# Kernel optimization log

Hardware: AMD Instinct MI355X
Metric: run time of the kernel (lower is better)

The kernel has to match this reference:

```python
import jax, jax.numpy as jnp
import numpy as np
from jax import lax

LENGTH = 9
PAD = LENGTH // 2          # 4
WIN_SIZE = LENGTH * LENGTH # 81
EPS = 1e-09
ALPHA = 0.01
PENALTY = 'l2'


def setup_inputs() -> dict:
    key = jax.random.key(0)
    k1, k2, k3 = jax.random.split(key, 3)
    B, C, H, W = 8, 1, 1024, 1024
    I = jax.random.normal(k1, (B, C, H, W), dtype=jnp.float32)
    J = jax.random.normal(k2, (B, C, H, W), dtype=jnp.float32)
    s = jax.random.normal(k3, (B, 2, H, W), dtype=jnp.float32)
    # buffer: all-ones box filter, shape [out=1, in=C, k, k]
    sum_filt = jnp.ones((1, C, LENGTH, LENGTH), dtype=jnp.float32)
    return {"I": I, "J": J, "s": s, "sum_filt": sum_filt}


def _box_conv(x, filt):
    # NCHW conv with 'same' padding (odd kernel), stride 1 -> [B,1,H,W]
    return lax.conv_general_dilated(
        x, filt, window_strides=(1, 1),
        padding=[(PAD, PAD), (PAD, PAD)],
        dimension_numbers=('NCHW', 'OIHW', 'NCHW'))


def _compute_local_sums(I, J, filt):
    I2, J2, IJ = I * I, J * J, I * J
    I_sum = _box_conv(I, filt)
    J_sum = _box_conv(J, filt)
    I2_sum = _box_conv(I2, filt)
    J2_sum = _box_conv(J2, filt)
    IJ_sum = _box_conv(IJ, filt)
    u_I = I_sum / WIN_SIZE
    u_J = J_sum / WIN_SIZE
    cross = IJ_sum - u_J * I_sum - u_I * J_sum + u_I * u_J * WIN_SIZE
    I_var = I2_sum - 2 * u_I * I_sum + u_I * u_I * WIN_SIZE
    J_var = J2_sum - 2 * u_J * J_sum + u_J * u_J * WIN_SIZE
    return I_var, J_var, cross


def _gradient_loss(s):
    dy = jnp.abs(s[:, :, 1:, :] - s[:, :, :-1, :])
    dx = jnp.abs(s[:, :, :, 1:] - s[:, :, :, :-1])
    if PENALTY == 'l2':
        dy = dy * dy
        dx = dx * dx
    return (jnp.mean(dx) + jnp.mean(dy)) / 2.0


def reference(I, J, s, sum_filt):
    I_var, J_var, cross = _compute_local_sums(I, J, sum_filt)
    cc = cross * cross / (I_var * J_var + EPS)
    ncc_loss = -jnp.mean(cc)
    smoothness_loss = _gradient_loss(s) * ALPHA
    total_loss = ncc_loss + smoothness_loss
    return (total_loss, ncc_loss, smoothness_loss)
```

## Files before the change

kernel.cpp:

```cpp
#include <hip/hip_runtime.h>

#define HH 1024
#define WW 1024
#define NB 8
#define TY 8
#define NCC_BLOCKS (NB * (HH / TY))
#define SROWS 16
#define SM_BLOCKS (NB * 2 * HH / SROWS)
#define RW (1.0f / 81.0f)

template <int SGN>
__device__ __forceinline__ void vrow(const float* __restrict__ Ib, const float* __restrict__ Jb,
                                     int y, int t,
                                     float vI[4], float vJ[4],
                                     float vI2[4], float vJ2[4], float vIJ[4]) {
    if (y < 0 || y >= HH) return;
    const float4 i4 = ((const float4*)(Ib + (size_t)y * WW))[t];
    const float4 j4 = ((const float4*)(Jb + (size_t)y * WW))[t];
    const float fi[4] = {i4.x, i4.y, i4.z, i4.w};
    const float fj[4] = {j4.x, j4.y, j4.z, j4.w};
#pragma unroll
    for (int c = 0; c < 4; ++c) {
        const float a = fi[c], b = fj[c];
        if (SGN > 0) {
            vI[c] += a; vJ[c] += b;
            vI2[c] = fmaf(a, a, vI2[c]);
            vJ2[c] = fmaf(b, b, vJ2[c]);
            vIJ[c] = fmaf(a, b, vIJ[c]);
        } else {
            vI[c] -= a; vJ[c] -= b;
            vI2[c] = fmaf(-a, a, vI2[c]);
            vJ2[c] = fmaf(-b, b, vJ2[c]);
            vIJ[c] = fmaf(-a, b, vIJ[c]);
        }
    }
}

__device__ __forceinline__ void hslide(const float4 l, const float4 r, const float own[4], float hs[4]) {
    float h = l.x + l.y + l.z + l.w + own[0] + own[1] + own[2] + own[3] + r.x;
    hs[0] = h;
    h += r.y - l.x; hs[1] = h;
    h += r.z - l.y; hs[2] = h;
    h += r.w - l.z; hs[3] = h;
}

__global__ __launch_bounds__(256) void fused_kernel(const float* __restrict__ I,
                                                    const float* __restrict__ J,
                                                    const float* __restrict__ S,
                                                    float* __restrict__ ws) {
    __shared__ float4 cs[5][258];
    __shared__ float red[8];
    const int bid = blockIdx.x;
    const int t = threadIdx.x;
    const int lane = t & 63;
    const int wid = t >> 6;

    if ((bid & 1) == 0) {
        const int nb = bid >> 1;
        const int b = nb >> 7;
        const int strip = nb & 127;
        const int y0 = strip * TY;
        const float* Ib = I + (size_t)b * HH * WW;
        const float* Jb = J + (size_t)b * HH * WW;

        float vI[4] = {0, 0, 0, 0}, vJ[4] = {0, 0, 0, 0};
        float vI2[4] = {0, 0, 0, 0}, vJ2[4] = {0, 0, 0, 0}, vIJ[4] = {0, 0, 0, 0};
        float ccacc = 0.f;

        if (t < 5) {
            cs[t][0] = float4{0, 0, 0, 0};
            cs[t][257] = float4{0, 0, 0, 0};
        }

#pragma unroll
        for (int k = 0; k < 8; ++k)
            vrow<1>(Ib, Jb, y0 - 4 + k, t, vI, vJ, vI2, vJ2, vIJ);

#pragma unroll 2
        for (int k = 0; k < TY; ++k) {
            const int y = y0 + k;
            vrow<1>(Ib, Jb, y + 4, t, vI, vJ, vI2, vJ2, vIJ);

            cs[0][t + 1] = float4{vI[0], vI[1], vI[2], vI[3]};
            cs[1][t + 1] = float4{vJ[0], vJ[1], vJ[2], vJ[3]};
            cs[2][t + 1] = float4{vI2[0], vI2[1], vI2[2], vI2[3]};
            cs[3][t + 1] = float4{vJ2[0], vJ2[1], vJ2[2], vJ2[3]};
            cs[4][t + 1] = float4{vIJ[0], vIJ[1], vIJ[2], vIJ[3]};
            __syncthreads();

            float hsI[4], hsJ[4], hsI2[4], hsJ2[4], hsIJ[4];
            hslide(cs[0][t], cs[0][t + 2], vI, hsI);
            hslide(cs[1][t], cs[1][t + 2], vJ, hsJ);
            hslide(cs[2][t], cs[2][t + 2], vI2, hsI2);
            hslide(cs[3][t], cs[3][t + 2], vJ2, hsJ2);
            hslide(cs[4][t], cs[4][t + 2], vIJ, hsIJ);
            __syncthreads();

#pragma unroll
            for (int c = 0; c < 4; ++c) {
                const float Is = hsI[c], Js = hsJ[c];
                const float cross = fmaf(-Is * Js, RW, hsIJ[c]);
                const float Iv = fmaf(-Is * Is, RW, hsI2[c]);
                const float Jv = fmaf(-Js * Js, RW, hsJ2[c]);
                const float den = fmaf(Iv, Jv, 1e-9f);
                ccacc += cross * cross * __builtin_amdgcn_rcpf(den);
            }

            vrow<-1>(Ib, Jb, y - 4, t, vI, vJ, vI2, vJ2, vIJ);
        }

#pragma unroll
        for (int o = 32; o; o >>= 1) ccacc += __shfl_down(ccacc, o);
        if (lane == 0) red[wid] = ccacc;
        __syncthreads();
        if (t == 0) ws[nb] = red[0] + red[1] + red[2] + red[3];
    } else {
        const int sb = bid >> 1;
        const int r0 = sb * SROWS;
        const float* base = S + (size_t)r0 * WW;
        float dxacc = 0.f, dyacc = 0.f;

        float4 v = ((const float4*)base)[t];
#pragma unroll 2
        for (int k = 0; k < SROWS; ++k) {
            const int y = (r0 + k) & (HH - 1);
            const float* rp = base + (size_t)k * WW;
            const float d0 = v.y - v.x, d1 = v.z - v.y, d2 = v.w - v.z;
            dxacc += d0 * d0 + d1 * d1 + d2 * d2;
            if (t < 255) { const float vr = rp[4 * t + 4]; const float d3 = vr - v.w; dxacc += d3 * d3; }
            if (y < HH - 1) {
                const float4 vn = ((const float4*)(rp + WW))[t];
                const float e0 = vn.x - v.x, e1 = vn.y - v.y, e2 = vn.z - v.z, e3 = vn.w - v.w;
                dyacc += e0 * e0 + e1 * e1 + e2 * e2 + e3 * e3;
                v = vn;
            }
        }

#pragma unroll
        for (int o = 32; o; o >>= 1) {
            dxacc += __shfl_down(dxacc, o);
            dyacc += __shfl_down(dyacc, o);
        }
        if (lane == 0) { red[wid] = dxacc; red[4 + wid] = dyacc; }
        __syncthreads();
        if (t == 0) {
            ws[NCC_BLOCKS + sb] = red[0] + red[1] + red[2] + red[3];
            ws[NCC_BLOCKS + SM_BLOCKS + sb] = red[4] + red[5] + red[6] + red[7];
        }
    }
}

__global__ __launch_bounds__(256) void finalize_kernel(const float* __restrict__ ws,
                                                       float* __restrict__ out) {
    __shared__ double sd[256];
    __shared__ double res[3];
    const int t = threadIdx.x;
    double cc = 0.0, dx = 0.0, dy = 0.0;
    for (int i = t; i < NCC_BLOCKS; i += 256) cc += (double)ws[i];
    for (int i = t; i < SM_BLOCKS; i += 256) dx += (double)ws[NCC_BLOCKS + i];
    for (int i = t; i < SM_BLOCKS; i += 256) dy += (double)ws[NCC_BLOCKS + SM_BLOCKS + i];

    sd[t] = cc; __syncthreads();
    for (int s = 128; s; s >>= 1) { if (t < s) sd[t] += sd[t + s]; __syncthreads(); }
    if (t == 0) res[0] = sd[0];
    __syncthreads();
    sd[t] = dx; __syncthreads();
    for (int s = 128; s; s >>= 1) { if (t < s) sd[t] += sd[t + s]; __syncthreads(); }
    if (t == 0) res[1] = sd[0];
    __syncthreads();
    sd[t] = dy; __syncthreads();
    for (int s = 128; s; s >>= 1) { if (t < s) sd[t] += sd[t + s]; __syncthreads(); }
    if (t == 0) {
        res[2] = sd[0];
        const double ncc = -(res[0] / ((double)NB * 1.0 * HH * WW));
        const double mdx = res[1] / ((double)NB * 2.0 * HH * (WW - 1));
        const double mdy = res[2] / ((double)NB * 2.0 * (HH - 1) * WW);
        const double smooth = 0.01 * 0.5 * (mdx + mdy);
        out[0] = (float)(ncc + smooth);
        out[1] = (float)ncc;
        out[2] = (float)smooth;
    }
}

extern "C" void kernel_launch(void* const* d_in, const int* in_sizes, int n_in,
                              void* d_out, int out_size, void* d_ws, size_t ws_size,
                              hipStream_t stream) {
    const float* I = (const float*)d_in[0];
    const float* J = (const float*)d_in[1];
    const float* S = (const float*)d_in[2];
    float* ws = (float*)d_ws;
    float* out = (float*)d_out;

    fused_kernel<<<NCC_BLOCKS + SM_BLOCKS, 256, 0, stream>>>(I, J, S, ws);
    finalize_kernel<<<1, 256, 0, stream>>>(ws, out);
}
```

Baseline: 182.5 us.

## Give each wave a full row strip with 16 columns per lane and shuffle halos

Each 64-lane wave now owns a whole 1024-column row strip of its own, with 16 columns per lane, instead of a 256-thread block sharing one strip. The horizontal 9-wide sums use wave shuffles for the halo columns in place of shared-memory column sums and two block barriers per row. The strip height drops to 4 rows and the grid interleaves NCC and smoothness blocks 2:1. Vertical halo re-reads per strip grow relative to useful rows, and register pressure rises because each lane keeps 80 accumulators.

```diff
diff --git a/kernel.cpp b/kernel.cpp
--- a/kernel.cpp
+++ b/kernel.cpp
@@ -3,136 +3,181 @@
 #define HH 1024
 #define WW 1024
 #define NB 8
-#define TY 8
-#define NCC_BLOCKS (NB * (HH / TY))
-#define SROWS 16
-#define SM_BLOCKS (NB * 2 * HH / SROWS)
+#define TY 4
+#define NCC_WAVES (NB * (HH / TY))
+#define NCC_BLOCKS (NCC_WAVES / 4)
+#define SM_BLOCKS 256
+#define GRID (NCC_BLOCKS + SM_BLOCKS)
 #define RW (1.0f / 81.0f)
 
 template <int SGN>
-__device__ __forceinline__ void vrow(const float* __restrict__ Ib, const float* __restrict__ Jb,
-                                     int y, int t,
-                                     float vI[4], float vJ[4],
-                                     float vI2[4], float vJ2[4], float vIJ[4]) {
+__device__ __forceinline__ void vrow16(const float* __restrict__ Ib, const float* __restrict__ Jb,
+                                       int y, int lane,
+                                       float vI[16], float vJ[16],
+                                       float vI2[16], float vJ2[16], float vIJ[16]) {
     if (y < 0 || y >= HH) return;
-    const float4 i4 = ((const float4*)(Ib + (size_t)y * WW))[t];
-    const float4 j4 = ((const float4*)(Jb + (size_t)y * WW))[t];
-    const float fi[4] = {i4.x, i4.y, i4.z, i4.w};
-    const float fj[4] = {j4.x, j4.y, j4.z, j4.w};
-#pragma unroll
-    for (int c = 0; c < 4; ++c) {
-        const float a = fi[c], b = fj[c];
-        if (SGN > 0) {
-            vI[c] += a; vJ[c] += b;
-            vI2[c] = fmaf(a, a, vI2[c]);
-            vJ2[c] = fmaf(b, b, vJ2[c]);
-            vIJ[c] = fmaf(a, b, vIJ[c]);
-        } else {
-            vI[c] -= a; vJ[c] -= b;
-            vI2[c] = fmaf(-a, a, vI2[c]);
-            vJ2[c] = fmaf(-b, b, vJ2[c]);
-            vIJ[c] = fmaf(-a, b, vIJ[c]);
+    const float4* Ir = (const float4*)(Ib + (size_t)y * WW) + 4 * lane;
+    const float4* Jr = (const float4*)(Jb + (size_t)y * WW) + 4 * lane;
+    float4 i4[4], j4[4];
+#pragma unroll
+    for (int k = 0; k < 4; ++k) i4[k] = Ir[k];
+#pragma unroll
+    for (int k = 0; k < 4; ++k) j4[k] = Jr[k];
+#pragma unroll
+    for (int k = 0; k < 4; ++k) {
+        const float fi[4] = {i4[k].x, i4[k].y, i4[k].z, i4[k].w};
+        const float fj[4] = {j4[k].x, j4[k].y, j4[k].z, j4[k].w};
+#pragma unroll
+        for (int e = 0; e < 4; ++e) {
+            const int c = 4 * k + e;
+            const float a = fi[e], b = fj[e];
+            if (SGN > 0) {
+                vI[c] += a; vJ[c] += b;
+                vI2[c] = fmaf(a, a, vI2[c]);
+                vJ2[c] = fmaf(b, b, vJ2[c]);
+                vIJ[c] = fmaf(a, b, vIJ[c]);
+            } else {
+                vI[c] -= a; vJ[c] -= b;
+                vI2[c] = fmaf(-a, a, vI2[c]);
+                vJ2[c] = fmaf(-b, b, vJ2[c]);
+                vIJ[c] = fmaf(-a, b, vIJ[c]);
+            }
         }
     }
-}
-
-__device__ __forceinline__ void hslide(const float4 l, const float4 r, const float own[4], float hs[4]) {
-    float h = l.x + l.y + l.z + l.w + own[0] + own[1] + own[2] + own[3] + r.x;
-    hs[0] = h;
-    h += r.y - l.x; hs[1] = h;
-    h += r.z - l.y; hs[2] = h;
-    h += r.w - l.z; hs[3] = h;
 }
 
 __global__ __launch_bounds__(256) void fused_kernel(const float* __restrict__ I,
                                                     const float* __restrict__ J,
                                                     const float* __restrict__ S,
                                                     float* __restrict__ ws) {
-    __shared__ float4 cs[5][258];
     __shared__ float red[8];
     const int bid = blockIdx.x;
     const int t = threadIdx.x;
     const int lane = t & 63;
     const int wid = t >> 6;
 
-    if ((bid & 1) == 0) {
-        const int nb = bid >> 1;
-        const int b = nb >> 7;
-        const int strip = nb & 127;
-        const int y0 = strip * TY;
+    if ((bid % 3) < 2) {
+        const int nblk = (bid / 3) * 2 + (bid % 3);
+        const int ss = nblk * 4 + wid;
+        const int b = ss >> 8;
+        const int y0 = (ss & 255) * TY;
         const float* Ib = I + (size_t)b * HH * WW;
         const float* Jb = J + (size_t)b * HH * WW;
 
-        float vI[4] = {0, 0, 0, 0}, vJ[4] = {0, 0, 0, 0};
-        float vI2[4] = {0, 0, 0, 0}, vJ2[4] = {0, 0, 0, 0}, vIJ[4] = {0, 0, 0, 0};
+        float vI[16], vJ[16], vI2[16], vJ2[16], vIJ[16];
+#pragma unroll
+        for (int c = 0; c < 16; ++c) { vI[c] = 0; vJ[c] = 0; vI2[c] = 0; vJ2[c] = 0; vIJ[c] = 0; }
         float ccacc = 0.f;
 
-        if (t < 5) {
-            cs[t][0] = float4{0, 0, 0, 0};
-            cs[t][257] = float4{0, 0, 0, 0};
-        }
-
 #pragma unroll
         for (int k = 0; k < 8; ++k)
-            vrow<1>(Ib, Jb, y0 - 4 + k, t, vI, vJ, vI2, vJ2, vIJ);
-
-#pragma unroll 2
+            vrow16<1>(Ib, Jb, y0 - 4 + k, lane, vI, vJ, vI2, vJ2, vIJ);
+
+#pragma unroll
         for (int k = 0; k < TY; ++k) {
             const int y = y0 + k;
-            vrow<1>(Ib, Jb, y + 4, t, vI, vJ, vI2, vJ2, vIJ);
-
-            cs[0][t + 1] = float4{vI[0], vI[1], vI[2], vI[3]};
-            cs[1][t + 1] = float4{vJ[0], vJ[1], vJ[2], vJ[3]};
-            cs[2][t + 1] = float4{vI2[0], vI2[1], vI2[2], vI2[3]};
-            cs[3][t + 1] = float4{vJ2[0], vJ2[1], vJ2[2], vJ2[3]};
-            cs[4][t + 1] = float4{vIJ[0], vIJ[1], vIJ[2], vIJ[3]};
-            __syncthreads();
-
-            float hsI[4], hsJ[4], hsI2[4], hsJ2[4], hsIJ[4];
-            hslide(cs[0][t], cs[0][t + 2], vI, hsI);
-            hslide(cs[1][t], cs[1][t + 2], vJ, hsJ);
-            hslide(cs[2][t], cs[2][t + 2], vI2, hsI2);
-            hslide(cs[3][t], cs[3][t + 2], vJ2, hsJ2);
-            hslide(cs[4][t], cs[4][t + 2], vIJ, hsIJ);
-            __syncthreads();
-
-#pragma unroll
-            for (int c = 0; c < 4; ++c) {
-                const float Is = hsI[c], Js = hsJ[c];
-                const float cross = fmaf(-Is * Js, RW, hsIJ[c]);
-                const float Iv = fmaf(-Is * Is, RW, hsI2[c]);
-                const float Jv = fmaf(-Js * Js, RW, hsJ2[c]);
+            vrow16<1>(Ib, Jb, y + 4, lane, vI, vJ, vI2, vJ2, vIJ);
+
+            float lI[4], lJ[4], lI2[4], lJ2[4], lIJ[4];
+            float rI[4], rJ[4], rI2[4], rJ2[4], rIJ[4];
+#pragma unroll
+            for (int j = 0; j < 4; ++j) {
+                lI[j] = __shfl_up(vI[12 + j], 1);
+                lJ[j] = __shfl_up(vJ[12 + j], 1);
+                lI2[j] = __shfl_up(vI2[12 + j], 1);
+                lJ2[j] = __shfl_up(vJ2[12 + j], 1);
+                lIJ[j] = __shfl_up(vIJ[12 + j], 1);
+                rI[j] = __shfl_down(vI[j], 1);
+                rJ[j] = __shfl_down(vJ[j], 1);
+                rI2[j] = __shfl_down(vI2[j], 1);
+                rJ2[j] = __shfl_down(vJ2[j], 1);
+                rIJ[j] = __shfl_down(vIJ[j], 1);
+            }
+            if (lane == 0) {
+#pragma unroll
+                for (int j = 0; j < 4; ++j) { lI[j] = 0; lJ[j] = 0; lI2[j] = 0; lJ2[j] = 0; lIJ[j] = 0; }
+            }
+            if (lane == 63) {
+#pragma unroll
+                for (int j = 0; j < 4; ++j) { rI[j] = 0; rJ[j] = 0; rI2[j] = 0; rJ2[j] = 0; rIJ[j] = 0; }
+            }
+
+            float wI = lI[0] + lI[1] + lI[2] + lI[3] + vI[0] + vI[1] + vI[2] + vI[3] + vI[4];
+            float wJ = lJ[0] + lJ[1] + lJ[2] + lJ[3] + vJ[0] + vJ[1] + vJ[2] + vJ[3] + vJ[4];
+            float wI2 = lI2[0] + lI2[1] + lI2[2] + lI2[3] + vI2[0] + vI2[1] + vI2[2] + vI2[3] + vI2[4];
+            float wJ2 = lJ2[0] + lJ2[1] + lJ2[2] + lJ2[3] + vJ2[0] + vJ2[1] + vJ2[2] + vJ2[3] + vJ2[4];
+            float wIJ = lIJ[0] + lIJ[1] + lIJ[2] + lIJ[3] + vIJ[0] + vIJ[1] + vIJ[2] + vIJ[3] + vIJ[4];
+
+#pragma unroll
+            for (int c = 0; c < 16; ++c) {
+                if (c > 0) {
+                    const float aI = (c < 12) ? vI[c + 4] : rI[c - 12];
+                    const float aJ = (c < 12) ? vJ[c + 4] : rJ[c - 12];
+                    const float aI2 = (c < 12) ? vI2[c + 4] : rI2[c - 12];
+                    const float aJ2 = (c < 12) ? vJ2[c + 4] : rJ2[c - 12];
+                    const float aIJ = (c < 12) ? vIJ[c + 4] : rIJ[c - 12];
+                    const float sI = (c >= 5) ? vI[c - 5] : lI[c - 1];
+                    const float sJ = (c >= 5) ? vJ[c - 5] : lJ[c - 1];
+                    const float sI2 = (c >= 5) ? vI2[c - 5] : lI2[c - 1];
+                    const float sJ2 = (c >= 5) ? vJ2[c - 5] : lJ2[c - 1];
+                    const float sIJ = (c >= 5) ? vIJ[c - 5] : lIJ[c - 1];
+                    wI += aI - sI; wJ += aJ - sJ;
+                    wI2 += aI2 - sI2; wJ2 += aJ2 - sJ2;
+                    wIJ += aIJ - sIJ;
+                }
+                const float t1 = wI * wJ;
+                const float cross = fmaf(-t1, RW, wIJ);
+                const float t2 = wI * wI;
+                const float Iv = fmaf(-t2, RW, wI2);
+                const float t3 = wJ * wJ;
+                const float Jv = fmaf(-t3, RW, wJ2);
                 const float den = fmaf(Iv, Jv, 1e-9f);
                 ccacc += cross * cross * __builtin_amdgcn_rcpf(den);
             }
 
-            vrow<-1>(Ib, Jb, y - 4, t, vI, vJ, vI2, vJ2, vIJ);
+            vrow16<-1>(Ib, Jb, y - 4, lane, vI, vJ, vI2, vJ2, vIJ);
         }
 
 #pragma unroll
         for (int o = 32; o; o >>= 1) ccacc += __shfl_down(ccacc, o);
         if (lane == 0) red[wid] = ccacc;
         __syncthreads();
-        if (t == 0) ws[nb] = red[0] + red[1] + red[2] + red[3];
+        if (t == 0) ws[nblk] = red[0] + red[1] + red[2] + red[3];
     } else {
-        const int sb = bid >> 1;
-        const int r0 = sb * SROWS;
+        const int sb = bid / 3;
+        const int r0 = sb * 64 + wid * 16;
         const float* base = S + (size_t)r0 * WW;
         float dxacc = 0.f, dyacc = 0.f;
 
-        float4 v = ((const float4*)base)[t];
+        float4 v[4];
+        {
+            const float4* rp4 = (const float4*)base + 4 * lane;
+#pragma unroll
+            for (int k = 0; k < 4; ++k) v[k] = rp4[k];
+        }
 #pragma unroll 2
-        for (int k = 0; k < SROWS; ++k) {
-            const int y = (r0 + k) & (HH - 1);
-            const float* rp = base + (size_t)k * WW;
-            const float d0 = v.y - v.x, d1 = v.z - v.y, d2 = v.w - v.z;
-            dxacc += d0 * d0 + d1 * d1 + d2 * d2;
-            if (t < 255) { const float vr = rp[4 * t + 4]; const float d3 = vr - v.w; dxacc += d3 * d3; }
-            if (y < HH - 1) {
-                const float4 vn = ((const float4*)(rp + WW))[t];
-                const float e0 = vn.x - v.x, e1 = vn.y - v.y, e2 = vn.z - v.z, e3 = vn.w - v.w;
-                dyacc += e0 * e0 + e1 * e1 + e2 * e2 + e3 * e3;
-                v = vn;
+        for (int k = 0; k < 16; ++k) {
+            const float f[16] = {v[0].x, v[0].y, v[0].z, v[0].w, v[1].x, v[1].y, v[1].z, v[1].w,
+                                 v[2].x, v[2].y, v[2].z, v[2].w, v[3].x, v[3].y, v[3].z, v[3].w};
+#pragma unroll
+            for (int c = 0; c < 15; ++c) { const float d = f[c + 1] - f[c]; dxacc = fmaf(d, d, dxacc); }
+            const float nb0 = __shfl_down(v[0].x, 1);
+            if (lane < 63) { const float d = nb0 - f[15]; dxacc = fmaf(d, d, dxacc); }
+
+            if (((r0 + k) & (HH - 1)) != HH - 1) {
+                const float4* np4 = (const float4*)(base + (size_t)(k + 1) * WW) + 4 * lane;
+                float4 nv[4];
+#pragma unroll
+                for (int q = 0; q < 4; ++q) nv[q] = np4[q];
+#pragma unroll
+                for (int q = 0; q < 4; ++q) {
+                    const float e0 = nv[q].x - v[q].x, e1 = nv[q].y - v[q].y;
+                    const float e2 = nv[q].z - v[q].z, e3 = nv[q].w - v[q].w;
+                    dyacc = fmaf(e0, e0, dyacc); dyacc = fmaf(e1, e1, dyacc);
+                    dyacc = fmaf(e2, e2, dyacc); dyacc = fmaf(e3, e3, dyacc);
+                }
+#pragma unroll
+                for (int q = 0; q < 4; ++q) v[q] = nv[q];
             }
         }
 
@@ -191,6 +236,6 @@
     float* ws = (float*)d_ws;
     float* out = (float*)d_out;
 
-    fused_kernel<<<NCC_BLOCKS + SM_BLOCKS, 256, 0, stream>>>(I, J, S, ws);
+    fused_kernel<<<GRID, 256, 0, stream>>>(I, J, S, ws);
     finalize_kernel<<<1, 256, 0, stream>>>(ws, out);
 }
```

After: 175.8 us. -3.6%, faster.
